# Kernel optimization log

Measured on AMD Instinct MI355X. Metric: run time of the kernel, lower is better.

Reference implementation:

```python
import jax, jax.numpy as jnp
import numpy as np

NNZ = 131072      # number of sparse 2-tuples
M = 1048576       # number of precomputed product triples for spspmm
EMB = 128


def _mlp(x, W0, b0, W1, b1):
    # MLP(emb_dim, emb_dim, mlplayer=2, tailact=True): linear+ReLU twice
    h = jax.nn.relu(x @ W0 + b0)
    return jax.nn.relu(h @ W1 + b1)


def setup_inputs() -> dict:
    key = jax.random.key(0)
    ks = jax.random.split(key, 8)
    s = 1.0 / np.sqrt(EMB)
    Xv = jax.random.normal(ks[0], (NNZ, EMB), dtype=jnp.float32)
    W1_0 = jax.random.normal(ks[1], (EMB, EMB), dtype=jnp.float32) * s
    W1_1 = jax.random.normal(ks[2], (EMB, EMB), dtype=jnp.float32) * s
    W2_0 = jax.random.normal(ks[3], (EMB, EMB), dtype=jnp.float32) * s
    W2_1 = jax.random.normal(ks[4], (EMB, EMB), dtype=jnp.float32) * s
    b = jnp.zeros((EMB,), dtype=jnp.float32)
    ind_a = jax.random.randint(ks[5], (M,), 0, NNZ, dtype=jnp.int32)
    ind_b = jax.random.randint(ks[6], (M,), 0, NNZ, dtype=jnp.int32)
    ind_out = jax.random.randint(ks[7], (M,), 0, NNZ, dtype=jnp.int32)
    return {"Xv": Xv, "W1_0": W1_0, "b1_0": b, "W1_1": W1_1, "b1_1": b,
            "W2_0": W2_0, "b2_0": b, "W2_1": W2_1, "b2_1": b,
            "ind_a": ind_a, "ind_b": ind_b, "ind_out": ind_out}


def reference(Xv, W1_0, b1_0, W1_1, b1_1, W2_0, b2_0, W2_1, b2_1,
              ind_a, ind_b, ind_out):
    # tuplewise MLP transforms
    X1 = _mlp(Xv, W1_0, b1_0, W1_1, b1_1)   # [nnz, emb]
    X2 = _mlp(Xv, W2_0, b2_0, W2_1, b2_1)   # [nnz, emb]
    # messagepassing_tuple with sum aggregation (sparse spspmm via
    # precomputed product triples): out[t] += X1[a] * X2[b]
    prod = X1[ind_a] * X2[ind_b]            # [M, emb]
    out = jax.ops.segment_sum(prod, ind_out, num_segments=NNZ)  # [nnz, emb]
    return out
```

## Files before the change

kernel.cpp:

```cpp
#include <hip/hip_runtime.h>
#include <hip/hip_bf16.h>

#define NNZ  131072
#define MT   1048576
#define EMB  128
#define NSEG 2048
#define SEGSZ 64
#define ENTCAP 1024

typedef __attribute__((ext_vector_type(8))) short  short8;
typedef __attribute__((ext_vector_type(4))) float  floatx4;

__device__ __forceinline__ ushort f2bf(float f) {
    unsigned u = __float_as_uint(f);
    u = (u + 0x7FFFu + ((u >> 16) & 1u)) >> 16;
    return (ushort)u;
}
__device__ __forceinline__ float bfl(unsigned u) { return __uint_as_float(u << 16); }
__device__ __forceinline__ float bfh(unsigned u) { return __uint_as_float(u & 0xffff0000u); }

__device__ __forceinline__ unsigned long long packE(int a, int b, int o) {
    return (unsigned long long)(unsigned)a |
           ((unsigned long long)(unsigned)b << 17) |
           ((unsigned long long)(unsigned)(o & 63) << 34);
}

__global__ __launch_bounds__(256) void prep_kernel(
    const float* __restrict__ W10, const float* __restrict__ W11,
    const float* __restrict__ W20, const float* __restrict__ W21,
    ushort* __restrict__ Wpk, const int* __restrict__ io,
    int* __restrict__ bh)
{
    __shared__ int h[NSEG];
    const int bid = blockIdx.x, tid = threadIdx.x;

    if (bid < 32) {
        int s = bid * 256 + tid;
        int L = s >> 11, sl = s & 2047;
        const float* W = (L == 0) ? W10 : (L == 1) ? W11 : (L == 2) ? W20 : W21;
        int lane = sl & 63, nk = sl >> 6;
        int col  = (nk >> 2) * 16 + (lane & 15);
        int krow = (nk & 3) * 32 + (lane >> 4) * 8;
        short8 w;
        #pragma unroll
        for (int j = 0; j < 8; ++j)
            w[j] = (short)f2bf(W[(krow + j) * EMB + col]);
        *(short8*)&Wpk[(size_t)s * 8] = w;
        return;
    }

    const int b = bid - 32;
    for (int i = tid; i < NSEG; i += 256) h[i] = 0;
    __syncthreads();
    const int4* io4 = (const int4*)io + b * 1024;
    for (int j = tid; j < 1024; j += 256) {
        int4 v = io4[j];
        atomicAdd(&h[v.x >> 6], 1);
        atomicAdd(&h[v.y >> 6], 1);
        atomicAdd(&h[v.z >> 6], 1);
        atomicAdd(&h[v.w >> 6], 1);
    }
    __syncthreads();
    for (int d = tid; d < NSEG; d += 256) bh[d * 256 + b] = h[d];
}

__global__ __launch_bounds__(256) void scanA_kernel(
    const int* __restrict__ bh, int* __restrict__ segtot)
{
    __shared__ int r[4];
    const int d = blockIdx.x, tid = threadIdx.x;
    int v = bh[d * 256 + tid];
    #pragma unroll
    for (int off = 32; off; off >>= 1) v += __shfl_down(v, off, 64);
    if ((tid & 63) == 0) r[tid >> 6] = v;
    __syncthreads();
    if (tid == 0) segtot[d] = r[0] + r[1] + r[2] + r[3];
}

__global__ __launch_bounds__(1024) void scanB_kernel(
    const int* __restrict__ segtot, int* __restrict__ segptr)
{
    __shared__ int part[1024];
    const int tid = threadIdx.x;
    int a = segtot[tid * 2], b = segtot[tid * 2 + 1];
    int s = a + b;
    part[tid] = s;
    __syncthreads();
    for (int off = 1; off < 1024; off <<= 1) {
        int v = (tid >= off) ? part[tid - off] : 0;
        __syncthreads();
        part[tid] += v;
        __syncthreads();
    }
    int run = part[tid] - s;
    segptr[tid * 2]     = run;
    segptr[tid * 2 + 1] = run + a;
    if (tid == 1023) segptr[NSEG] = run + s;
}

__global__ __launch_bounds__(256) void scanC_kernel(
    int* __restrict__ bh, const int* __restrict__ segptr)
{
    __shared__ int wsum[4];
    const int d = blockIdx.x, tid = threadIdx.x;
    int v = bh[d * 256 + tid];
    int pfx = v;
    #pragma unroll
    for (int off = 1; off < 64; off <<= 1) {
        int t = __shfl_up(pfx, off, 64);
        if ((tid & 63) >= off) pfx += t;
    }
    if ((tid & 63) == 63) wsum[tid >> 6] = pfx;
    __syncthreads();
    int wb = 0;
    #pragma unroll
    for (int w = 0; w < 4; ++w) if (w < (tid >> 6)) wb += wsum[w];
    bh[d * 256 + tid] = segptr[d] + wb + pfx - v;
}

__global__ __launch_bounds__(256, 3) void union_kernel(
    const float* __restrict__ Xv, const ushort* __restrict__ Wpk,
    const float* __restrict__ b10, const float* __restrict__ b11,
    const float* __restrict__ b20, const float* __restrict__ b21,
    ushort* __restrict__ X1b, ushort* __restrict__ X2b,
    const int* __restrict__ io, const int* __restrict__ ia,
    const int* __restrict__ ib, const int* __restrict__ bh,
    unsigned long long* __restrict__ srt)
{
    __shared__ ushort Wp[16384];
    __shared__ ushort Hs[8192];

    const int bid = blockIdx.x;
    const int tid = threadIdx.x;
    const int q   = bid / 9;

    if (bid == q * 9) {
        int* cur = (int*)Wp;
        for (int d = tid; d < NSEG; d += 256) cur[d] = bh[d * 256 + q];
        __syncthreads();
        const int4* io4 = (const int4*)io + q * 1024;
        const int4* ia4 = (const int4*)ia + q * 1024;
        const int4* ib4 = (const int4*)ib + q * 1024;
        for (int j = tid; j < 1024; j += 256) {
            int4 o = io4[j], a = ia4[j], c = ib4[j];
            int p;
            p = atomicAdd(&cur[o.x >> 6], 1); srt[p] = packE(a.x, c.x, o.x);
            p = atomicAdd(&cur[o.y >> 6], 1); srt[p] = packE(a.y, c.y, o.y);
            p = atomicAdd(&cur[o.z >> 6], 1); srt[p] = packE(a.z, c.z, o.z);
            p = atomicAdd(&cur[o.w >> 6], 1); srt[p] = packE(a.w, c.w, o.w);
        }
        return;
    }

    const int mid  = bid - q - 1;
    const int wave = tid >> 6;
    const int lane = tid & 63;
    const int g    = lane >> 4;
    const int r    = lane & 15;
    const int rowbase = mid * 64 + wave * 16;
    char* hw = (char*)(Hs + wave * 2048);

    short8 af[4];
    {
        const float* xsrc = Xv + (size_t)(rowbase + r) * EMB;
        #pragma unroll
        for (int kt = 0; kt < 4; ++kt) {
            const float4* p = (const float4*)(xsrc + kt * 32 + g * 8);
            float4 v0 = p[0], v1 = p[1];
            short8 a;
            a[0] = (short)f2bf(v0.x); a[1] = (short)f2bf(v0.y);
            a[2] = (short)f2bf(v0.z); a[3] = (short)f2bf(v0.w);
            a[4] = (short)f2bf(v1.x); a[5] = (short)f2bf(v1.y);
            a[6] = (short)f2bf(v1.z); a[7] = (short)f2bf(v1.w);
            af[kt] = a;
        }
    }

    auto stageW = [&](int L) {
        const ushort* src = Wpk + (size_t)L * 16384;
        #pragma unroll
        for (int s = tid; s < 2048; s += 256)
            *(short8*)&Wp[s * 8] = *(const short8*)&src[(size_t)s * 8];
    };

    floatx4 acc[8];
    auto runMFMA = [&](const short8* a4) {
        #pragma unroll
        for (int n = 0; n < 8; ++n) {
            floatx4 c = {0.f, 0.f, 0.f, 0.f};
            #pragma unroll
            for (int kt = 0; kt < 4; ++kt) {
                short8 b = *(const short8*)&Wp[((n * 4 + kt) * 64 + lane) * 8];
                c = __builtin_amdgcn_mfma_f32_16x16x32_bf16(b, a4[kt], c, 0, 0, 0);
            }
            acc[n] = c;
        }
    };

    auto epi = [&](const float* __restrict__ bias) {
        #pragma unroll
        for (int n = 0; n < 8; ++n) {
            float4 bv = *(const float4*)&bias[n * 16 + g * 4];
            ushort4 w;
            w.x = f2bf(fmaxf(acc[n][0] + bv.x, 0.f));
            w.y = f2bf(fmaxf(acc[n][1] + bv.y, 0.f));
            w.z = f2bf(fmaxf(acc[n][2] + bv.z, 0.f));
            w.w = f2bf(fmaxf(acc[n][3] + bv.w, 0.f));
            int byte = r * 256 + n * 32 + g * 8;
            byte ^= ((r & 3) << 5) ^ ((r & 4) << 2);
            *(ushort4*)(hw + byte) = w;
        }
    };

    auto loadH = [&](short8* h4) {
        #pragma unroll
        for (int kt = 0; kt < 4; ++kt) {
            int byte = r * 256 + kt * 64 + g * 16;
            byte ^= ((r & 3) << 5) ^ ((r & 4) << 2);
            h4[kt] = *(const short8*)(hw + byte);
        }
    };

    auto storeG = [&](ushort* __restrict__ dst) {
        #pragma unroll
        for (int it = 0; it < 4; ++it) {
            int row  = it * 4 + g;
            int byte = row * 256 + (lane & 15) * 16;
            byte ^= ((row & 3) << 5) ^ ((row & 4) << 2);
            short8 v = *(const short8*)(hw + byte);
            *(short8*)&dst[(size_t)rowbase * EMB + row * EMB + (lane & 15) * 8] = v;
        }
    };

    short8 h4[4];

    stageW(0); __syncthreads();
    runMFMA(af); epi(b10); __syncthreads();
    stageW(1); loadH(h4); __syncthreads();
    runMFMA(h4); epi(b11); __syncthreads();
    stageW(2); storeG(X1b); __syncthreads();
    runMFMA(af); epi(b20); __syncthreads();
    stageW(3); loadH(h4); __syncthreads();
    runMFMA(h4); epi(b21); __syncthreads();
    storeG(X2b);
}

__global__ __launch_bounds__(1024, 2) void gather_seg(
    const ushort* __restrict__ X1b, const ushort* __restrict__ X2b,
    const unsigned long long* __restrict__ srt, const int* __restrict__ segptr,
    float* __restrict__ out)
{
    __shared__ unsigned long long ent[ENTCAP];
    __shared__ unsigned long long sorted[ENTCAP];
    __shared__ int hist[64];
    __shared__ int rptr[65];

    const int s   = blockIdx.x;
    const int tid = threadIdx.x;

    const int beg = segptr[s], end = segptr[s + 1];
    const int n  = end - beg;
    const int nl = n > ENTCAP ? ENTCAP : n;

    if (tid < 64) hist[tid] = 0;
    __syncthreads();

    for (int i = tid; i < nl; i += 1024) {
        unsigned long long e = srt[beg + i];
        ent[i] = e;
        atomicAdd(&hist[(int)(e >> 34)], 1);
    }
    __syncthreads();

    if (tid < 64) {
        int c = hist[tid];
        int pfx = c;
        #pragma unroll
        for (int off = 1; off < 64; off <<= 1) {
            int v = __shfl_up(pfx, off, 64);
            if (tid >= off) pfx += v;
        }
        rptr[tid] = pfx - c;
        hist[tid] = pfx - c;
        if (tid == 63) rptr[64] = pfx;
    }
    __syncthreads();

    for (int i = tid; i < nl; i += 1024) {
        unsigned long long e = ent[i];
        int p = atomicAdd(&hist[(int)(e >> 34)], 1);
        sorted[p] = e;
    }
    __syncthreads();

    const int wv = tid >> 6, lane = tid & 63;
    const unsigned* x1 = (const unsigned*)X1b + lane;
    const unsigned* x2 = (const unsigned*)X2b + lane;

    #pragma unroll
    for (int rr = 0; rr < 4; ++rr) {
        const int row = wv * 4 + rr;
        const int rb = rptr[row], re = rptr[row + 1];
        float ax = 0.f, ay = 0.f;
        for (int c = rb; c < re; c += 8) {
            int m = re - c; if (m > 8) m = 8;
            unsigned long long E[8];
            #pragma unroll
            for (int e = 0; e < 8; ++e)
                E[e] = sorted[c + (e < m ? e : 0)];
            #pragma unroll
            for (int e = 0; e < 8; ++e) {
                unsigned u1 = x1[(unsigned)(E[e] & 0x1FFFF) * 64u];
                unsigned u2 = x2[(unsigned)((E[e] >> 17) & 0x1FFFF) * 64u];
                if (e >= m) u1 = 0u;
                ax += bfl(u1) * bfl(u2);
                ay += bfh(u1) * bfh(u2);
            }
        }
        if (n > ENTCAP) {
            for (int i = beg + ENTCAP; i < end; ++i) {
                unsigned long long e = srt[i];
                if ((int)(e >> 34) == row) {
                    unsigned u1 = x1[(unsigned)(e & 0x1FFFF) * 64u];
                    unsigned u2 = x2[(unsigned)((e >> 17) & 0x1FFFF) * 64u];
                    ax += bfl(u1) * bfl(u2);
                    ay += bfh(u1) * bfh(u2);
                }
            }
        }
        *(float2*)(out + ((size_t)s * SEGSZ + row) * EMB + lane * 2) =
            make_float2(ax, ay);
    }
}

extern "C" void kernel_launch(void* const* d_in, const int* in_sizes, int n_in,
                              void* d_out, int out_size, void* d_ws, size_t ws_size,
                              hipStream_t stream)
{
    (void)in_sizes; (void)n_in; (void)out_size; (void)ws_size;

    const float* Xv  = (const float*)d_in[0];
    const float* W10 = (const float*)d_in[1];
    const float* b10 = (const float*)d_in[2];
    const float* W11 = (const float*)d_in[3];
    const float* b11 = (const float*)d_in[4];
    const float* W20 = (const float*)d_in[5];
    const float* b20 = (const float*)d_in[6];
    const float* W21 = (const float*)d_in[7];
    const float* b21 = (const float*)d_in[8];
    const int*   ia  = (const int*)d_in[9];
    const int*   ib  = (const int*)d_in[10];
    const int*   io  = (const int*)d_in[11];
    float* out = (float*)d_out;

    char* ws = (char*)d_ws;
    ushort*             X1b    = (ushort*)(ws);
    ushort*             X2b    = (ushort*)(ws + 33554432);
    ushort*             Wpk    = (ushort*)(ws + 67108864);
    int*                bh     = (int*)(ws + 67371008);
    int*                segptr = (int*)(ws + 69468160);
    int*                segtot = (int*)(ws + 69484544);
    unsigned long long* srt    = (unsigned long long*)(ws + 69763072);

    prep_kernel<<<288, 256, 0, stream>>>(W10, W11, W20, W21, Wpk, io, bh);
    scanA_kernel<<<NSEG, 256, 0, stream>>>(bh, segtot);
    scanB_kernel<<<1, 1024, 0, stream>>>(segtot, segptr);
    scanC_kernel<<<NSEG, 256, 0, stream>>>(bh, segptr);
    union_kernel<<<2304, 256, 0, stream>>>(Xv, Wpk, b10, b11, b20, b21,
                                           X1b, X2b, io, ia, ib, bh, srt);
    gather_seg<<<NSEG, 1024, 0, stream>>>(X1b, X2b, srt, segptr, out);
}
```

Baseline: 156.7 us.

## Split gather into fixed-width bucket pass plus overflow side list

Splits the segment gather into three kernels. A sort kernel writes each output row's first 16 (a,b) pairs into a fixed-width bucket padded with a zero row. A branch-free gather kernel then reads those 16 pairs for every row, and a single-block side-fix kernel applies overflow entries with atomics. The aim is to remove the irregular per-row loop lengths and load imbalance of the old gather. In exchange it adds a bucket round-trip through global memory, two extra launches, and wasted loads on padding entries. The side list is capped at a fixed size, and the old handling of segments with more than 1024 entries is gone, so overflow beyond either cap would be silently dropped.

```diff
diff --git a/kernel.cpp b/kernel.cpp
--- a/kernel.cpp
+++ b/kernel.cpp
@@ -7,6 +7,8 @@
 #define NSEG 2048
 #define SEGSZ 64
 #define ENTCAP 1024
+#define ZR   131072
+#define SIDECAP 16384
 
 typedef __attribute__((ext_vector_type(8))) short  short8;
 typedef __attribute__((ext_vector_type(4))) float  floatx4;
@@ -29,7 +31,8 @@
     const float* __restrict__ W10, const float* __restrict__ W11,
     const float* __restrict__ W20, const float* __restrict__ W21,
     ushort* __restrict__ Wpk, const int* __restrict__ io,
-    int* __restrict__ bh)
+    int* __restrict__ bh, ushort* __restrict__ X1b, ushort* __restrict__ X2b,
+    int* __restrict__ sideCnt)
 {
     __shared__ int h[NSEG];
     const int bid = blockIdx.x, tid = threadIdx.x;
@@ -50,6 +53,14 @@
     }
 
     const int b = bid - 32;
+    if (b == 0) {
+        if (tid < 32) {
+            int4* dst = (tid < 16) ? (int4*)&X1b[(size_t)ZR * EMB]
+                                   : (int4*)&X2b[(size_t)ZR * EMB];
+            dst[tid & 15] = make_int4(0, 0, 0, 0);
+        }
+        if (tid == 32) *sideCnt = 0;
+    }
     for (int i = tid; i < NSEG; i += 256) h[i] = 0;
     __syncthreads();
     const int4* io4 = (const int4*)io + b * 1024;
@@ -245,10 +256,10 @@
     storeG(X2b);
 }
 
-__global__ __launch_bounds__(1024, 2) void gather_seg(
-    const ushort* __restrict__ X1b, const ushort* __restrict__ X2b,
+__global__ __launch_bounds__(1024, 2) void sort_seg(
     const unsigned long long* __restrict__ srt, const int* __restrict__ segptr,
-    float* __restrict__ out)
+    int2* __restrict__ bucket, unsigned long long* __restrict__ sideList,
+    int* __restrict__ sideCnt)
 {
     __shared__ unsigned long long ent[ENTCAP];
     __shared__ unsigned long long sorted[ENTCAP];
@@ -257,24 +268,20 @@
 
     const int s   = blockIdx.x;
     const int tid = threadIdx.x;
-
     const int beg = segptr[s], end = segptr[s + 1];
     const int n  = end - beg;
     const int nl = n > ENTCAP ? ENTCAP : n;
 
     if (tid < 64) hist[tid] = 0;
     __syncthreads();
-
     for (int i = tid; i < nl; i += 1024) {
         unsigned long long e = srt[beg + i];
         ent[i] = e;
         atomicAdd(&hist[(int)(e >> 34)], 1);
     }
     __syncthreads();
-
     if (tid < 64) {
-        int c = hist[tid];
-        int pfx = c;
+        int c = hist[tid], pfx = c;
         #pragma unroll
         for (int off = 1; off < 64; off <<= 1) {
             int v = __shfl_up(pfx, off, 64);
@@ -285,7 +292,6 @@
         if (tid == 63) rptr[64] = pfx;
     }
     __syncthreads();
-
     for (int i = tid; i < nl; i += 1024) {
         unsigned long long e = ent[i];
         int p = atomicAdd(&hist[(int)(e >> 34)], 1);
@@ -293,43 +299,70 @@
     }
     __syncthreads();
 
-    const int wv = tid >> 6, lane = tid & 63;
+    for (int i = tid; i < nl; i += 1024) {
+        unsigned long long e = sorted[i];
+        int row  = (int)(e >> 34);
+        int rank = i - rptr[row];
+        int a = (int)(e & 0x1FFFF), b = (int)((e >> 17) & 0x1FFFF);
+        int go = (s << 6) + row;
+        if (rank < 16) {
+            bucket[((size_t)go << 4) + rank] = make_int2(a, b);
+        } else {
+            int idx = atomicAdd(sideCnt, 1);
+            if (idx < SIDECAP)
+                sideList[idx] = (unsigned long long)(unsigned)a |
+                                ((unsigned long long)(unsigned)b << 17) |
+                                ((unsigned long long)(unsigned)go << 34);
+        }
+    }
+    {
+        int row = tid >> 4, k = tid & 15;
+        int cnt = rptr[row + 1] - rptr[row];
+        if (k >= cnt)
+            bucket[((size_t)((s << 6) + row) << 4) + k] = make_int2(ZR, ZR);
+    }
+}
+
+__global__ __launch_bounds__(256) void gather_b(
+    const ushort* __restrict__ X1b, const ushort* __restrict__ X2b,
+    const int2* __restrict__ bucket, float* __restrict__ out)
+{
+    int o    = blockIdx.x * 4 + (threadIdx.x >> 6);
+    int lane = threadIdx.x & 63;
     const unsigned* x1 = (const unsigned*)X1b + lane;
     const unsigned* x2 = (const unsigned*)X2b + lane;
 
+    int2 P[16];
     #pragma unroll
-    for (int rr = 0; rr < 4; ++rr) {
-        const int row = wv * 4 + rr;
-        const int rb = rptr[row], re = rptr[row + 1];
-        float ax = 0.f, ay = 0.f;
-        for (int c = rb; c < re; c += 8) {
-            int m = re - c; if (m > 8) m = 8;
-            unsigned long long E[8];
-            #pragma unroll
-            for (int e = 0; e < 8; ++e)
-                E[e] = sorted[c + (e < m ? e : 0)];
-            #pragma unroll
-            for (int e = 0; e < 8; ++e) {
-                unsigned u1 = x1[(unsigned)(E[e] & 0x1FFFF) * 64u];
-                unsigned u2 = x2[(unsigned)((E[e] >> 17) & 0x1FFFF) * 64u];
-                if (e >= m) u1 = 0u;
-                ax += bfl(u1) * bfl(u2);
-                ay += bfh(u1) * bfh(u2);
-            }
-        }
-        if (n > ENTCAP) {
-            for (int i = beg + ENTCAP; i < end; ++i) {
-                unsigned long long e = srt[i];
-                if ((int)(e >> 34) == row) {
-                    unsigned u1 = x1[(unsigned)(e & 0x1FFFF) * 64u];
-                    unsigned u2 = x2[(unsigned)((e >> 17) & 0x1FFFF) * 64u];
-                    ax += bfl(u1) * bfl(u2);
-                    ay += bfh(u1) * bfh(u2);
-                }
-            }
-        }
-        *(float2*)(out + ((size_t)s * SEGSZ + row) * EMB + lane * 2) =
-            make_float2(ax, ay);
+    for (int e = 0; e < 16; ++e) P[e] = bucket[((size_t)o << 4) + e];
+
+    float ax = 0.f, ay = 0.f;
+    #pragma unroll
+    for (int e = 0; e < 16; ++e) {
+        unsigned u1 = x1[(unsigned)P[e].x * 64u];
+        unsigned u2 = x2[(unsigned)P[e].y * 64u];
+        ax += bfl(u1) * bfl(u2);
+        ay += bfh(u1) * bfh(u2);
+    }
+    *(float2*)(out + (size_t)o * EMB + lane * 2) = make_float2(ax, ay);
+}
+
+__global__ __launch_bounds__(1024) void side_fix(
+    const ushort* __restrict__ X1b, const ushort* __restrict__ X2b,
+    const unsigned long long* __restrict__ sideList,
+    const int* __restrict__ sideCnt, float* __restrict__ out)
+{
+    int m = *sideCnt; if (m > SIDECAP) m = SIDECAP;
+    int wv = threadIdx.x >> 6, lane = threadIdx.x & 63;
+    for (int i = wv; i < m; i += 16) {
+        unsigned long long e = sideList[i];
+        int a   = (int)(e & 0x1FFFF);
+        int b   = (int)((e >> 17) & 0x1FFFF);
+        int row = (int)(e >> 34);
+        unsigned u1 = *((const unsigned*)X1b + lane + (unsigned)a * 64u);
+        unsigned u2 = *((const unsigned*)X2b + lane + (unsigned)b * 64u);
+        atomicAdd(out + (size_t)row * EMB + lane * 2,     bfl(u1) * bfl(u2));
+        atomicAdd(out + (size_t)row * EMB + lane * 2 + 1, bfh(u1) * bfh(u2));
     }
 }
 
@@ -355,18 +388,24 @@
 
     char* ws = (char*)d_ws;
     ushort*             X1b    = (ushort*)(ws);
-    ushort*             X2b    = (ushort*)(ws + 33554432);
-    ushort*             Wpk    = (ushort*)(ws + 67108864);
-    int*                bh     = (int*)(ws + 67371008);
-    int*                segptr = (int*)(ws + 69468160);
-    int*                segtot = (int*)(ws + 69484544);
-    unsigned long long* srt    = (unsigned long long*)(ws + 69763072);
-
-    prep_kernel<<<288, 256, 0, stream>>>(W10, W11, W20, W21, Wpk, io, bh);
+    ushort*             X2b    = (ushort*)(ws + 33554688);
+    ushort*             Wpk    = (ushort*)(ws + 67109376);
+    int*                bh     = (int*)(ws + 67371520);
+    int*                segtot = (int*)(ws + 69468672);
+    int*                segptr = (int*)(ws + 69485056);
+    int*                sideCnt= (int*)(ws + 69501440);
+    unsigned long long* sideList=(unsigned long long*)(ws + 69501568);
+    unsigned long long* srt    = (unsigned long long*)(ws + 69632640);
+    int2*               bucket = (int2*)(ws + 78021248);
+
+    prep_kernel<<<288, 256, 0, stream>>>(W10, W11, W20, W21, Wpk, io, bh,
+                                         X1b, X2b, sideCnt);
     scanA_kernel<<<NSEG, 256, 0, stream>>>(bh, segtot);
     scanB_kernel<<<1, 1024, 0, stream>>>(segtot, segptr);
     scanC_kernel<<<NSEG, 256, 0, stream>>>(bh, segptr);
     union_kernel<<<2304, 256, 0, stream>>>(Xv, Wpk, b10, b11, b20, b21,
                                            X1b, X2b, io, ia, ib, bh, srt);
-    gather_seg<<<NSEG, 1024, 0, stream>>>(X1b, X2b, srt, segptr, out);
-}
+    sort_seg<<<NSEG, 1024, 0, stream>>>(srt, segptr, bucket, sideList, sideCnt);
+    gather_b<<<NNZ / 4, 256, 0, stream>>>(X1b, X2b, bucket, out);
+    side_fix<<<1, 1024, 0, stream>>>(X1b, X2b, sideList, sideCnt, out);
+}
```

Measured after the change: 204.1 us. 1.3x slower.

## Replace per-segment row sort with fixed-point LDS atomic accumulation in gather

Applied to the files above, without the earlier changes.

The gather kernel no longer builds a per-row histogram, prefix scan and counting sort of each segment's entries in shared memory. Each wave now takes chunks of entries straight from global memory and adds the products, converted to fixed point with a 2^16 scale, into a shared int accumulator with integer atomics. This drops several barriers and the sort phases and removes the overflow path for oversized segments. The cost is LDS atomic contention and rounding to 1/65536 with possible int overflow for large sums, which can hurt accuracy.

```diff
diff --git a/kernel.cpp b/kernel.cpp
--- a/kernel.cpp
+++ b/kernel.cpp
@@ -6,7 +6,6 @@
 #define EMB  128
 #define NSEG 2048
 #define SEGSZ 64
-#define ENTCAP 1024
 
 typedef __attribute__((ext_vector_type(8))) short  short8;
 typedef __attribute__((ext_vector_type(4))) float  floatx4;
@@ -245,91 +244,58 @@
     storeG(X2b);
 }
 
-__global__ __launch_bounds__(1024, 2) void gather_seg(
+__global__ __launch_bounds__(1024, 2) void gather_fx(
     const ushort* __restrict__ X1b, const ushort* __restrict__ X2b,
     const unsigned long long* __restrict__ srt, const int* __restrict__ segptr,
     float* __restrict__ out)
 {
-    __shared__ unsigned long long ent[ENTCAP];
-    __shared__ unsigned long long sorted[ENTCAP];
-    __shared__ int hist[64];
-    __shared__ int rptr[65];
-
+    __shared__ int acc[SEGSZ][2][64];
     const int s   = blockIdx.x;
     const int tid = threadIdx.x;
+    const int wv  = tid >> 6, lane = tid & 63;
+
+    int4 z4 = make_int4(0, 0, 0, 0);
+    ((int4*)acc)[tid * 2]     = z4;
+    ((int4*)acc)[tid * 2 + 1] = z4;
+    __syncthreads();
 
     const int beg = segptr[s], end = segptr[s + 1];
-    const int n  = end - beg;
-    const int nl = n > ENTCAP ? ENTCAP : n;
-
-    if (tid < 64) hist[tid] = 0;
-    __syncthreads();
-
-    for (int i = tid; i < nl; i += 1024) {
-        unsigned long long e = srt[beg + i];
-        ent[i] = e;
-        atomicAdd(&hist[(int)(e >> 34)], 1);
-    }
-    __syncthreads();
-
-    if (tid < 64) {
-        int c = hist[tid];
-        int pfx = c;
-        #pragma unroll
-        for (int off = 1; off < 64; off <<= 1) {
-            int v = __shfl_up(pfx, off, 64);
-            if (tid >= off) pfx += v;
-        }
-        rptr[tid] = pfx - c;
-        hist[tid] = pfx - c;
-        if (tid == 63) rptr[64] = pfx;
-    }
-    __syncthreads();
-
-    for (int i = tid; i < nl; i += 1024) {
-        unsigned long long e = ent[i];
-        int p = atomicAdd(&hist[(int)(e >> 34)], 1);
-        sorted[p] = e;
-    }
-    __syncthreads();
-
-    const int wv = tid >> 6, lane = tid & 63;
+    const int n = end - beg;
     const unsigned* x1 = (const unsigned*)X1b + lane;
     const unsigned* x2 = (const unsigned*)X2b + lane;
-
+    const float SC = 65536.0f;
+
+    for (int c = wv * 8; c < n; c += 128) {
+        int m = n - c; if (m > 8) m = 8;
+        unsigned long long E[8];
+        #pragma unroll
+        for (int e = 0; e < 8; ++e)
+            E[e] = srt[beg + c + (e < m ? e : 0)];
+        #pragma unroll
+        for (int e = 0; e < 8; ++e) {
+            unsigned u1 = x1[(unsigned)(E[e] & 0x1FFFF) * 64u];
+            unsigned u2 = x2[(unsigned)((E[e] >> 17) & 0x1FFFF) * 64u];
+            int ro = (int)(E[e] >> 34);
+            if (e >= m) u1 = 0u;
+            int p0 = __float2int_rn(bfl(u1) * bfl(u2) * SC);
+            int p1 = __float2int_rn(bfh(u1) * bfh(u2) * SC);
+            atomicAdd(&acc[ro][0][lane], p0);
+            atomicAdd(&acc[ro][1][lane], p1);
+        }
+    }
+    __syncthreads();
+
+    const float inv = 1.0f / 65536.0f;
     #pragma unroll
-    for (int rr = 0; rr < 4; ++rr) {
-        const int row = wv * 4 + rr;
-        const int rb = rptr[row], re = rptr[row + 1];
-        float ax = 0.f, ay = 0.f;
-        for (int c = rb; c < re; c += 8) {
-            int m = re - c; if (m > 8) m = 8;
-            unsigned long long E[8];
-            #pragma unroll
-            for (int e = 0; e < 8; ++e)
-                E[e] = sorted[c + (e < m ? e : 0)];
-            #pragma unroll
-            for (int e = 0; e < 8; ++e) {
-                unsigned u1 = x1[(unsigned)(E[e] & 0x1FFFF) * 64u];
-                unsigned u2 = x2[(unsigned)((E[e] >> 17) & 0x1FFFF) * 64u];
-                if (e >= m) u1 = 0u;
-                ax += bfl(u1) * bfl(u2);
-                ay += bfh(u1) * bfh(u2);
-            }
-        }
-        if (n > ENTCAP) {
-            for (int i = beg + ENTCAP; i < end; ++i) {
-                unsigned long long e = srt[i];
-                if ((int)(e >> 34) == row) {
-                    unsigned u1 = x1[(unsigned)(e & 0x1FFFF) * 64u];
-                    unsigned u2 = x2[(unsigned)((e >> 17) & 0x1FFFF) * 64u];
-                    ax += bfl(u1) * bfl(u2);
-                    ay += bfh(u1) * bfh(u2);
-                }
-            }
-        }
-        *(float2*)(out + ((size_t)s * SEGSZ + row) * EMB + lane * 2) =
-            make_float2(ax, ay);
+    for (int h = 0; h < 2; ++h) {
+        int t   = tid + h * 1024;
+        int row = t >> 5, qq = t & 31;
+        float4 v;
+        v.x = acc[row][0][2 * qq]     * inv;
+        v.y = acc[row][1][2 * qq]     * inv;
+        v.z = acc[row][0][2 * qq + 1] * inv;
+        v.w = acc[row][1][2 * qq + 1] * inv;
+        *(float4*)(out + ((size_t)s * SEGSZ + row) * EMB + qq * 4) = v;
     }
 }
 
@@ -368,5 +334,5 @@
     scanC_kernel<<<NSEG, 256, 0, stream>>>(bh, segptr);
     union_kernel<<<2304, 256, 0, stream>>>(Xv, Wpk, b10, b11, b20, b21,
                                            X1b, X2b, io, ia, ib, bh, srt);
-    gather_seg<<<NSEG, 1024, 0, stream>>>(X1b, X2b, srt, segptr, out);
-}
+    gather_fx<<<NSEG, 1024, 0, stream>>>(X1b, X2b, srt, segptr, out);
+}
```

Result: slower. 165.8 us (+5.8%).
